# Performance work log

Hardware: AMD Instinct MI355X
Metric: run time of the kernel (lower is better)

## Reference

```python
import jax, jax.numpy as jnp
import numpy as np

B, N, PREV, PRED, H = 16, 64, 6, 30, 256
E = N * (N - 1)
BN_EPS = 1e-5


def _mlp(x, W1, b1, W2, b2, gamma, beta):
    # Two-layer ELU MLP with batch norm over flattened (batch*rows) dim.
    h = jax.nn.elu(x @ W1 + b1)
    h = jax.nn.elu(h @ W2 + b2)
    b, n, d = h.shape
    f = h.reshape(b * n, d)
    mu = f.mean(axis=0)
    var = f.var(axis=0)
    f = (f - mu) * jax.lax.rsqrt(var + BN_EPS) * gamma + beta
    return f.reshape(b, n, d)


def setup_inputs() -> dict:
    key = jax.random.key(0)
    ks = jax.random.split(key, 8)
    # fully-connected directed graph without self loops
    recv, send = np.where(~np.eye(N, dtype=bool))  # each [E]
    rel_rec = jnp.broadcast_to(jax.nn.one_hot(jnp.asarray(recv), N)[None], (B, E, N)).astype(jnp.float32)
    rel_send = jnp.broadcast_to(jax.nn.one_hot(jnp.asarray(send), N)[None], (B, E, N)).astype(jnp.float32)

    def xavier(k, shape):
        fan_in, fan_out = shape
        std = np.sqrt(2.0 / (fan_in + fan_out))
        return jax.random.normal(k, shape, jnp.float32) * std

    return {
        "prev_actor_centers": jax.random.normal(ks[0], (B, N, PREV, 2), jnp.float32) * 10.0,
        "rel_rec": rel_rec,
        "rel_send": rel_send,
        "W_traj": xavier(ks[1], (PREV * 2, H)),
        "b_traj": jnp.full((H,), 0.1, jnp.float32),
        "n2e_W1": xavier(ks[2], (2 * H, H)),
        "n2e_b1": jnp.full((H,), 0.1, jnp.float32),
        "n2e_W2": xavier(ks[3], (H, H)),
        "n2e_b2": jnp.full((H,), 0.1, jnp.float32),
        "n2e_gamma": jnp.ones((H,), jnp.float32),
        "n2e_beta": jnp.zeros((H,), jnp.float32),
        "e2n_W1": xavier(ks[4], (2 * H, H)),
        "e2n_b1": jnp.full((H,), 0.1, jnp.float32),
        "e2n_W2": xavier(ks[5], (H, H)),
        "e2n_b2": jnp.full((H,), 0.1, jnp.float32),
        "e2n_gamma": jnp.ones((H,), jnp.float32),
        "e2n_beta": jnp.zeros((H,), jnp.float32),
        "W_fuse": xavier(ks[6], (2 * H, H)),
        "b_fuse": jnp.full((H,), 0.1, jnp.float32),
        "W_pred": xavier(ks[7], (H, PRED * 2)),
        "b_pred": jnp.full((PRED * 2,), 0.1, jnp.float32),
    }


def reference(prev_actor_centers, rel_rec, rel_send,
              W_traj, b_traj,
              n2e_W1, n2e_b1, n2e_W2, n2e_b2, n2e_gamma, n2e_beta,
              e2n_W1, e2n_b1, e2n_W2, e2n_b2, e2n_gamma, e2n_beta,
              W_fuse, b_fuse, W_pred, b_pred):
    b, n, prev, _ = prev_actor_centers.shape
    # relative displacements, first step zero
    diffs = prev_actor_centers[:, :, 1:, :] - prev_actor_centers[:, :, :-1, :]
    rel_pos = jnp.concatenate([jnp.zeros((b, n, 1, 2), prev_actor_centers.dtype), diffs], axis=2)
    rel_pos = rel_pos.reshape(b, n, prev * 2)
    x = rel_pos @ W_traj + b_traj  # [b, n, H] node features

    # node2edge: gather via one-hot relation matmuls
    receivers = jnp.einsum('ben,bnh->beh', rel_rec, x)
    senders = jnp.einsum('ben,bnh->beh', rel_send, x)
    edges = jnp.concatenate([receivers, senders], axis=-1)  # [b, E, 2H]
    e = _mlp(edges, n2e_W1, n2e_b1, n2e_W2, n2e_b2, n2e_gamma, n2e_beta)

    # edge2node: degree-normalized scatter via transposed relation matmuls
    deg_rec = rel_rec.sum(axis=1)  # [b, n]
    deg_rec = deg_rec + (deg_rec == 0).astype(deg_rec.dtype)
    incoming = jnp.einsum('ben,beh->bnh', rel_rec, e) / deg_rec[..., None]
    deg_send = rel_send.sum(axis=1)
    deg_send = deg_send + (deg_send == 0).astype(deg_send.dtype)
    outgoing = jnp.einsum('ben,beh->bnh', rel_send, e) / deg_send[..., None]
    nodes = jnp.concatenate([incoming, outgoing], axis=-1)  # [b, n, 2H]
    m = _mlp(nodes, e2n_W1, e2n_b1, e2n_W2, e2n_b2, e2n_gamma, e2n_beta)

    fused = jnp.concatenate([x, m], axis=-1) @ W_fuse + b_fuse  # [b, n, H]
    rel = fused @ W_pred + b_pred  # [b, n, PRED*2]

    current_loc = prev_actor_centers[:, :, -1, :]  # [b, n, 2]
    current_loc = jnp.broadcast_to(current_loc[:, :, None, :], (b, n, PRED, 2)).reshape(b, n, PRED * 2)
    pos = jnp.cumsum(rel.reshape(b, n, PRED, 2), axis=2).reshape(b, n, PRED * 2) + current_loc
    return (rel, pos)
```

## Files before the change

### kernel.cpp

```cpp
#include <hip/hip_runtime.h>
#include <hip/hip_bf16.h>

#define BB 16
#define NN 64
#define PREVN 6
#define PREDN 30
#define HH 256
#define EE 4032
#define EROWS (BB*EE)
#define NROWS (BB*NN)

typedef short short8 __attribute__((ext_vector_type(8)));
typedef float f32x4 __attribute__((ext_vector_type(4)));

enum : int {
  OFF_STATS_E = 0,
  OFF_STATS_M = 1024,
  OFF_XRS     = 2048,
  F32_END     = 264192
};
enum : size_t {
  BO_W1TE  = 0,
  BO_W2TE  = 131072,
  BO_W1TN  = 196608,
  BO_W2TN  = 327680,
  BO_WFT   = 393216,
  BO_WPT   = 524288,
  BO_XG    = 540672,
  BO_NODES = 802816,
  BO_H1G   = 1327104,
  BO_M2    = 1589248,
  BO_FG    = 1851392,
  BO_E2    = 2113536
};

__device__ __forceinline__ float eluf(float v) { return v > 0.f ? v : __expf(v) - 1.f; }

__device__ __forceinline__ float xembed(const float* __restrict__ centers,
                                        const float* __restrict__ Wt,
                                        const float* __restrict__ bt,
                                        int rr, int col) {
  const float* c = centers + rr * 12;
  float acc = bt[col];
  #pragma unroll
  for (int t = 0; t < 5; ++t) {
    float dx = c[(t+1)*2 + 0] - c[t*2 + 0];
    float dy = c[(t+1)*2 + 1] - c[t*2 + 1];
    acc += dx * Wt[(2 + 2*t)*HH + col] + dy * Wt[(3 + 2*t)*HH + col];
  }
  return acc;
}

struct PrepArgs {
  const float *centers, *W_traj, *b_traj;
  const float *n2e_W1, *n2e_W2, *e2n_W1, *e2n_W2, *W_fuse, *W_pred;
  float* ws;
  float* inc;
  __hip_bfloat16 *p1e, *p2e, *p1n, *p2n, *pf, *pp, *xg;
};

__global__ __launch_bounds__(256) void k_prep(PrepArgs a) {
  const int bid = blockIdx.x, tid = threadIdx.x;
  if (bid < 264) {
    const float* W; __hip_bfloat16* P; int ksh, t0, pad = 0;
    if (bid < 64)       { W = a.n2e_W1; P = a.p1e; ksh = 4; t0 = bid*4; }
    else if (bid < 96)  { W = a.n2e_W2; P = a.p2e; ksh = 3; t0 = (bid-64)*4; }
    else if (bid < 160) { W = a.e2n_W1; P = a.p1n; ksh = 4; t0 = (bid-96)*4; }
    else if (bid < 192) { W = a.e2n_W2; P = a.p2n; ksh = 3; t0 = (bid-160)*4; }
    else if (bid < 256) { W = a.W_fuse; P = a.pf;  ksh = 4; t0 = (bid-192)*4; }
    else                { W = a.W_pred; P = a.pp;  ksh = 3; t0 = (bid-256)*4; pad = 1; }
    const int l = tid & 63, sub = tid >> 6;
    const int t = t0 + sub;
    const int j = t >> ksh, ks = t & ((1 << ksh) - 1);
    const int m16 = l & 15, q = l >> 4;
    __hip_bfloat16* dst = P + ((size_t)t*64 + l)*8;
    if (!pad) {
      const float* src = W + (size_t)(ks*32 + q*8)*256 + j*16 + m16;
      #pragma unroll
      for (int e = 0; e < 8; ++e)
        dst[e] = __float2bfloat16(src[(size_t)e*256]);
    } else {
      const int col = j*16 + m16;
      #pragma unroll
      for (int e = 0; e < 8; ++e)
        dst[e] = __float2bfloat16(col < 60 ?
                     W[(size_t)(ks*32 + q*8 + e)*60 + col] : 0.f);
    }
  } else if (bid < 272) {
    a.ws[(bid - 264) * 256 + tid] = 0.f;
  } else if (bid < 336) {
    int row0 = (bid - 272) * 16;
    #pragma unroll
    for (int r = 0; r < 16; ++r)
      a.xg[(size_t)(row0 + r)*256 + tid] =
          __float2bfloat16(xembed(a.centers, a.W_traj, a.b_traj, row0 + r, tid));
  } else {
    float* p = a.inc + (size_t)(bid - 336) * 4096;
    #pragma unroll
    for (int i = 0; i < 4; ++i)
      *reinterpret_cast<float4*>(p + (i*256 + tid)*4) = (float4){0.f,0.f,0.f,0.f};
  }
}

__global__ __launch_bounds__(64) void k_xrs2(
    const __hip_bfloat16* __restrict__ xg,
    const __hip_bfloat16* __restrict__ W1P,
    const float* __restrict__ b1,
    __hip_bfloat16* __restrict__ xrs) {
  const int lane = threadIdx.x;
  const int m16 = lane & 15, quad = lane >> 4;
  const int ko = quad * 8;
  const int rt = blockIdx.x >> 3, s = blockIdx.x & 7;
  const int half = s >> 2, j0 = (s & 3) * 64;
  const int jg0 = (s & 3) * 4;
  const int row0 = rt * 16;
  __hip_bfloat16* dst = xrs + (size_t)half * 262144;

  f32x4 acc[4];
  #pragma unroll
  for (int jt = 0; jt < 4; ++jt) {
    float bv = half ? 0.f : b1[j0 + jt*16 + m16];
    acc[jt] = (f32x4){bv, bv, bv, bv};
  }
  #pragma unroll
  for (int ks = 0; ks < 8; ++ks) {
    short8 af = *reinterpret_cast<const short8*>(
        xg + (size_t)(row0 + m16)*256 + ks*32 + ko);
    short8 bf[4];
    #pragma unroll
    for (int jt = 0; jt < 4; ++jt)
      bf[jt] = *reinterpret_cast<const short8*>(
          W1P + (((size_t)(jg0 + jt)*16 + half*8 + ks)*64 + lane)*8);
    #pragma unroll
    for (int jt = 0; jt < 4; ++jt)
      acc[jt] = __builtin_amdgcn_mfma_f32_16x16x32_bf16(af, bf[jt], acc[jt], 0, 0, 0);
  }
  #pragma unroll
  for (int jt = 0; jt < 4; ++jt)
    #pragma unroll
    for (int r = 0; r < 4; ++r)
      dst[(size_t)(row0 + quad*4 + r)*256 + j0 + jt*16 + m16] =
          __float2bfloat16(acc[jt][r]);
}

__global__ __launch_bounds__(256, 4) void k_mlp8(
    const __hip_bfloat16* __restrict__ xrs,
    const __hip_bfloat16* __restrict__ W2P,
    const float* __restrict__ b2,
    __hip_bfloat16* __restrict__ outp,
    float* __restrict__ stats,
    float* __restrict__ incraw) {
  __shared__ alignas(16) __hip_bfloat16 h1s[64][264];
  __shared__ float sst[3][256];
  const int tid = threadIdx.x;
  const int w = tid >> 6, lane = tid & 63;
  const int m16 = lane & 15, quad = lane >> 4;
  const int ko = quad * 8;
  const int blk = blockIdx.x;
  const int bb = blk / 63, lb = blk - bb*63;
  const int n0 = (lb * 64) / 63;
  const int thr = (n0 + 1) * 63 - lb * 64;
  const int colw = w * 64;

  #pragma unroll
  for (int i = 0; i < 3; ++i) sst[i][tid] = 0.f;

  {
    const int rg = tid >> 5;
    const int c8 = (tid & 31) * 8;
    const __hip_bfloat16* xrb = xrs + (size_t)(bb*64 + n0)*256 + c8;
    const __hip_bfloat16* xsb = xrs + 262144 + (size_t)bb*64*256 + c8;
    union { uint4 u; __hip_bfloat16 h[8]; } vr0, vr1;
    vr0.u = *reinterpret_cast<const uint4*>(xrb);
    vr1.u = *reinterpret_cast<const uint4*>(xrb + 256);
    #pragma unroll
    for (int i = 0; i < 8; ++i) {
      int r = rg + i*8;
      int isn1 = (r >= thr) ? 1 : 0;
      int rc = n0 + isn1;
      int jj = lb*64 + r - rc*63;
      int sd = jj + (jj >= rc ? 1 : 0);
      union { uint4 u; __hip_bfloat16 h[8]; } vs, va, o;
      vs.u = *reinterpret_cast<const uint4*>(xsb + (size_t)sd*256);
      va.u = isn1 ? vr1.u : vr0.u;
      #pragma unroll
      for (int j = 0; j < 8; ++j)
        o.h[j] = __float2bfloat16(eluf(__bfloat162float(va.h[j]) +
                                       __bfloat162float(vs.h[j])));
      *reinterpret_cast<uint4*>(&h1s[r][c8]) = o.u;
    }
  }
  __syncthreads();

  f32x4 acc2[4][4];
  #pragma unroll
  for (int jt = 0; jt < 4; ++jt) {
    float bv = b2[colw + jt*16 + m16];
    #pragma unroll
    for (int mt = 0; mt < 4; ++mt) acc2[mt][jt] = (f32x4){bv, bv, bv, bv};
  }
  #pragma unroll
  for (int kt = 0; kt < 4; ++kt) {
    #pragma unroll
    for (int ks = 0; ks < 2; ++ks) {
      const int k0 = kt*64 + ks*32 + ko;
      const int chunk = kt*2 + ks;
      short8 af[4], bf[4];
      #pragma unroll
      for (int jt = 0; jt < 4; ++jt)
        bf[jt] = *reinterpret_cast<const short8*>(
            W2P + (((size_t)(w*4 + jt)*8 + chunk)*64 + lane)*8);
      #pragma unroll
      for (int mt = 0; mt < 4; ++mt)
        af[mt] = *(const short8*)((const char*)h1s +
                     (size_t)(mt*16 + m16)*528 + k0*2);
      #pragma unroll
      for (int mt = 0; mt < 4; ++mt)
        #pragma unroll
        for (int jt = 0; jt < 4; ++jt)
          acc2[mt][jt] = __builtin_amdgcn_mfma_f32_16x16x32_bf16(af[mt], bf[jt],
                                                                 acc2[mt][jt], 0, 0, 0);
    }
  }
  __syncthreads();

  #pragma unroll
  for (int jt = 0; jt < 4; ++jt) {
    float s0 = 0.f, s1 = 0.f, sq = 0.f;
    #pragma unroll
    for (int mt = 0; mt < 4; ++mt)
      #pragma unroll
      for (int r = 0; r < 4; ++r) {
        int row = mt*16 + quad*4 + r;
        float hv = eluf(acc2[mt][jt][r]);
        h1s[row][colw + jt*16 + m16] = __float2bfloat16(hv);
        float t1 = (row >= thr) ? hv : 0.f;
        s1 += t1; s0 += hv - t1;
        sq += hv * hv;
      }
    atomicAdd(&sst[0][colw + jt*16 + m16], s0);
    atomicAdd(&sst[1][colw + jt*16 + m16], s1);
    atomicAdd(&sst[2][colw + jt*16 + m16], sq);
  }
  __syncthreads();

  {
    float s0 = sst[0][tid], s1 = sst[1][tid];
    atomicAdd(&stats[tid], s0 + s1);
    atomicAdd(&stats[256 + tid], sst[2][tid]);
    atomicAdd(&incraw[(size_t)(bb*64 + n0)*256 + tid], s0);
    atomicAdd(&incraw[(size_t)(bb*64 + n0 + 1)*256 + tid], s1);
  }
  #pragma unroll
  for (int i = 0; i < 8; ++i) {
    int u = i*256 + tid;
    int r = u >> 5, c = (u & 31) * 8;
    int isn1 = (r >= thr) ? 1 : 0;
    int rc = n0 + isn1;
    int jj = lb*64 + r - rc*63;
    int sd = jj + (jj >= rc ? 1 : 0);
    int jpos = rc - (jj < rc ? 1 : 0);
    *reinterpret_cast<uint4*>(outp + ((size_t)(bb*64 + sd)*63 + jpos)*HH + c) =
        *reinterpret_cast<const uint4*>(&h1s[r][c]);
  }
}

__global__ __launch_bounds__(256) void k_aggS(const __hip_bfloat16* __restrict__ e2,
                                              const float* __restrict__ incraw,
                                              const float* __restrict__ st,
                                              const float* __restrict__ gam,
                                              const float* __restrict__ bet,
                                              __hip_bfloat16* __restrict__ nodes) {
  __shared__ float red[8][256];
  const int bn = blockIdx.x;
  const int tid = threadIdx.x;
  const int c8 = (tid & 31) * 8;
  const int rg = tid >> 5;
  const __hip_bfloat16* base = e2 + (size_t)bn * 63 * HH;
  float s[8] = {0.f,0.f,0.f,0.f,0.f,0.f,0.f,0.f};
  for (int j = rg; j < 63; j += 8) {
    union { uint4 u; __hip_bfloat16 h[8]; } v;
    v.u = *reinterpret_cast<const uint4*>(base + (size_t)j*HH + c8);
    #pragma unroll
    for (int jj = 0; jj < 8; ++jj) s[jj] += __bfloat162float(v.h[jj]);
  }
  #pragma unroll
  for (int jj = 0; jj < 8; jj += 4)
    *reinterpret_cast<float4*>(&red[rg][c8 + jj]) =
        (float4){s[jj], s[jj+1], s[jj+2], s[jj+3]};
  __syncthreads();
  float S = 0.f;
  #pragma unroll
  for (int r = 0; r < 8; ++r) S += red[r][tid];
  const float inv = 1.f / (float)EROWS;
  float mean = st[tid] * inv;
  float var  = fmaxf(st[256 + tid] * inv - mean*mean, 0.f);
  float a = gam[tid] * rsqrtf(var + 1e-5f);
  float c0 = bet[tid] - mean * a;
  float in_v  = a * (incraw[(size_t)bn*256 + tid] * (1.f/63.f)) + c0;
  float out_v = a * (S * (1.f/63.f)) + c0;
  nodes[(size_t)bn*512 + tid]       = __float2bfloat16(in_v);
  nodes[(size_t)bn*512 + 256 + tid] = __float2bfloat16(out_v);
}

__global__ __launch_bounds__(64) void k_n1(
    const __hip_bfloat16* __restrict__ nodes,
    const __hip_bfloat16* __restrict__ W1P,
    const float* __restrict__ b1,
    __hip_bfloat16* __restrict__ h1g) {
  __shared__ alignas(16) __hip_bfloat16 hls[16][40];
  const int lane = threadIdx.x;
  const int m16 = lane & 15, quad = lane >> 4;
  const int ko = quad * 8;
  const int row0 = (blockIdx.x >> 3) * 16;
  const int jb = blockIdx.x & 7;
  const int j0 = jb * 32;

  f32x4 acc[2];
  #pragma unroll
  for (int jt = 0; jt < 2; ++jt) {
    float bv = b1[j0 + jt*16 + m16];
    acc[jt] = (f32x4){bv, bv, bv, bv};
  }
  #pragma unroll
  for (int ks = 0; ks < 16; ++ks) {
    short8 af = *reinterpret_cast<const short8*>(
        nodes + (size_t)(row0 + m16)*512 + ks*32 + ko);
    short8 bf[2];
    #pragma unroll
    for (int jt = 0; jt < 2; ++jt)
      bf[jt] = *reinterpret_cast<const short8*>(
          W1P + (((size_t)(jb*2 + jt)*16 + ks)*64 + lane)*8);
    #pragma unroll
    for (int jt = 0; jt < 2; ++jt)
      acc[jt] = __builtin_amdgcn_mfma_f32_16x16x32_bf16(af, bf[jt], acc[jt], 0, 0, 0);
  }
  #pragma unroll
  for (int jt = 0; jt < 2; ++jt)
    #pragma unroll
    for (int r = 0; r < 4; ++r)
      hls[quad*4 + r][jt*16 + m16] = __float2bfloat16(eluf(acc[jt][r]));
  {
    int r = lane >> 2, c = (lane & 3) * 8;
    *reinterpret_cast<uint4*>(h1g + (size_t)(row0 + r)*256 + j0 + c) =
        *reinterpret_cast<const uint4*>(&hls[r][c]);
  }
}

__global__ __launch_bounds__(64) void k_n2(
    const __hip_bfloat16* __restrict__ h1g,
    const __hip_bfloat16* __restrict__ W2P,
    const float* __restrict__ b2,
    __hip_bfloat16* __restrict__ m2,
    float* __restrict__ stats) {
  __shared__ alignas(16) __hip_bfloat16 hls[16][40];
  __shared__ float sst[2][32];
  const int lane = threadIdx.x;
  const int m16 = lane & 15, quad = lane >> 4;
  const int ko = quad * 8;
  const int row0 = (blockIdx.x >> 3) * 16;
  const int jb = blockIdx.x & 7;
  const int j0 = jb * 32;

  if (lane < 32) { sst[0][lane] = 0.f; sst[1][lane] = 0.f; }

  f32x4 acc[2];
  #pragma unroll
  for (int jt = 0; jt < 2; ++jt) {
    float bv = b2[j0 + jt*16 + m16];
    acc[jt] = (f32x4){bv, bv, bv, bv};
  }
  #pragma unroll
  for (int ks = 0; ks < 8; ++ks) {
    short8 af = *reinterpret_cast<const short8*>(
        h1g + (size_t)(row0 + m16)*256 + ks*32 + ko);
    short8 bf[2];
    #pragma unroll
    for (int jt = 0; jt < 2; ++jt)
      bf[jt] = *reinterpret_cast<const short8*>(
          W2P + (((size_t)(jb*2 + jt)*8 + ks)*64 + lane)*8);
    #pragma unroll
    for (int jt = 0; jt < 2; ++jt)
      acc[jt] = __builtin_amdgcn_mfma_f32_16x16x32_bf16(af, bf[jt], acc[jt], 0, 0, 0);
  }
  #pragma unroll
  for (int jt = 0; jt < 2; ++jt) {
    float ps = 0.f, pq = 0.f;
    #pragma unroll
    for (int r = 0; r < 4; ++r) {
      float hv = eluf(acc[jt][r]);
      hls[quad*4 + r][jt*16 + m16] = __float2bfloat16(hv);
      ps += hv; pq += hv * hv;
    }
    atomicAdd(&sst[0][jt*16 + m16], ps);
    atomicAdd(&sst[1][jt*16 + m16], pq);
  }
  if (lane < 32) {
    atomicAdd(&stats[j0 + lane], sst[0][lane]);
    atomicAdd(&stats[256 + j0 + lane], sst[1][lane]);
  }
  {
    int r = lane >> 2, c = (lane & 3) * 8;
    *reinterpret_cast<uint4*>(m2 + (size_t)(row0 + r)*256 + j0 + c) =
        *reinterpret_cast<const uint4*>(&hls[r][c]);
  }
}

__global__ __launch_bounds__(64) void k_hf(
    const __hip_bfloat16* __restrict__ xg,
    const __hip_bfloat16* __restrict__ m2,
    const float* __restrict__ stM,
    const float* __restrict__ gam,
    const float* __restrict__ bet,
    const __hip_bfloat16* __restrict__ WfP,
    const float* __restrict__ bfv,
    __hip_bfloat16* __restrict__ fg) {
  __shared__ alignas(16) __hip_bfloat16 hls[16][40];
  __shared__ float bnA[256], bnC[256];
  const int lane = threadIdx.x;
  const int m16 = lane & 15, quad = lane >> 4;
  const int ko = quad * 8;
  const int row0 = (blockIdx.x >> 3) * 16;
  const int jb = blockIdx.x & 7;
  const int j0 = jb * 32;

  {
    const float inv = 1.f / (float)NROWS;
    #pragma unroll
    for (int j = 0; j < 4; ++j) {
      int k = lane*4 + j;
      float mean = stM[k] * inv;
      float var  = fmaxf(stM[256 + k] * inv - mean*mean, 0.f);
      float am = gam[k] * rsqrtf(var + 1e-5f);
      bnA[k] = am;
      bnC[k] = bet[k] - mean * am;
    }
  }

  f32x4 acc[2];
  #pragma unroll
  for (int jt = 0; jt < 2; ++jt) {
    float bv = bfv[j0 + jt*16 + m16];
    acc[jt] = (f32x4){bv, bv, bv, bv};
  }
  #pragma unroll
  for (int ks = 0; ks < 16; ++ks) {
    short8 af;
    if (ks < 8) {
      af = *reinterpret_cast<const short8*>(
          xg + (size_t)(row0 + m16)*256 + ks*32 + ko);
    } else {
      int k0 = (ks - 8)*32 + ko;
      union { uint4 u; __hip_bfloat16 h[8]; } v;
      v.u = *reinterpret_cast<const uint4*>(m2 + (size_t)(row0 + m16)*256 + k0);
      union { short8 s8; __hip_bfloat16 h[8]; } o;
      #pragma unroll
      for (int j = 0; j < 8; ++j)
        o.h[j] = __float2bfloat16(bnA[k0+j] * __bfloat162float(v.h[j]) + bnC[k0+j]);
      af = o.s8;
    }
    short8 bf[2];
    #pragma unroll
    for (int jt = 0; jt < 2; ++jt)
      bf[jt] = *reinterpret_cast<const short8*>(
          WfP + (((size_t)(jb*2 + jt)*16 + ks)*64 + lane)*8);
    #pragma unroll
    for (int jt = 0; jt < 2; ++jt)
      acc[jt] = __builtin_amdgcn_mfma_f32_16x16x32_bf16(af, bf[jt], acc[jt], 0, 0, 0);
  }
  #pragma unroll
  for (int jt = 0; jt < 2; ++jt)
    #pragma unroll
    for (int r = 0; r < 4; ++r)
      hls[quad*4 + r][jt*16 + m16] = __float2bfloat16(acc[jt][r]);
  {
    int r = lane >> 2, c = (lane & 3) * 8;
    *reinterpret_cast<uint4*>(fg + (size_t)(row0 + r)*256 + j0 + c) =
        *reinterpret_cast<const uint4*>(&hls[r][c]);
  }
}

__global__ __launch_bounds__(64) void k_pred(
    const __hip_bfloat16* __restrict__ fg,
    const __hip_bfloat16* __restrict__ WpP,
    const float* __restrict__ bp,
    const float* __restrict__ centers,
    float* __restrict__ out) {
  __shared__ float rl[16][68];
  const int lane = threadIdx.x;
  const int m16 = lane & 15, quad = lane >> 4;
  const int ko = quad * 8;
  const int row0 = blockIdx.x * 16;

  f32x4 acc[4];
  #pragma unroll
  for (int jt = 0; jt < 4; ++jt) {
    int c = jt*16 + m16;
    float bv = (c < 60) ? bp[c] : 0.f;
    acc[jt] = (f32x4){bv, bv, bv, bv};
  }
  #pragma unroll
  for (int ks = 0; ks < 8; ++ks) {
    short8 af = *reinterpret_cast<const short8*>(
        fg + (size_t)(row0 + m16)*256 + ks*32 + ko);
    short8 bf[4];
    #pragma unroll
    for (int jt = 0; jt < 4; ++jt)
      bf[jt] = *reinterpret_cast<const short8*>(
          WpP + (((size_t)jt*8 + ks)*64 + lane)*8);
    #pragma unroll
    for (int jt = 0; jt < 4; ++jt)
      acc[jt] = __builtin_amdgcn_mfma_f32_16x16x32_bf16(af, bf[jt], acc[jt], 0, 0, 0);
  }
  #pragma unroll
  for (int jt = 0; jt < 4; ++jt) {
    int c = jt*16 + m16;
    #pragma unroll
    for (int r = 0; r < 4; ++r) {
      int lr = quad*4 + r;
      rl[lr][c] = acc[jt][r];
      if (c < 60) out[(size_t)(row0 + lr)*60 + c] = acc[jt][r];
    }
  }
  if (lane < 32) {
    int lr = lane >> 1, xy = lane & 1;
    int grow = row0 + lr;
    float run = centers[(size_t)(grow*PREVN + 5)*2 + xy];
    #pragma unroll
    for (int p = 0; p < PREDN; ++p) {
      run += rl[lr][2*p + xy];
      out[61440 + (size_t)grow*60 + 2*p + xy] = run;
    }
  }
}

extern "C" void kernel_launch(void* const* d_in, const int* in_sizes, int n_in,
                              void* d_out, int out_size, void* d_ws, size_t ws_size,
                              hipStream_t stream) {
  const float* centers = (const float*)d_in[0];
  float* ws = (float*)d_ws;
  __hip_bfloat16* wb = (__hip_bfloat16*)(ws + F32_END);
  __hip_bfloat16* xrs = (__hip_bfloat16*)(ws + OFF_XRS);
  float* incraw = (float*)(wb + BO_H1G);

  const float* W_traj = (const float*)d_in[3];
  const float* b_traj = (const float*)d_in[4];
  const float* n2e_b1 = (const float*)d_in[6];
  const float* n2e_b2 = (const float*)d_in[8];
  const float* n2e_g  = (const float*)d_in[9];
  const float* n2e_be = (const float*)d_in[10];
  const float* e2n_b1 = (const float*)d_in[12];
  const float* e2n_b2 = (const float*)d_in[14];
  const float* e2n_g  = (const float*)d_in[15];
  const float* e2n_be = (const float*)d_in[16];
  const float* b_fuse = (const float*)d_in[18];
  const float* b_pred = (const float*)d_in[20];

  PrepArgs pa;
  pa.centers = centers; pa.W_traj = W_traj; pa.b_traj = b_traj;
  pa.n2e_W1 = (const float*)d_in[5];  pa.n2e_W2 = (const float*)d_in[7];
  pa.e2n_W1 = (const float*)d_in[11]; pa.e2n_W2 = (const float*)d_in[13];
  pa.W_fuse = (const float*)d_in[17]; pa.W_pred = (const float*)d_in[19];
  pa.ws = ws; pa.inc = incraw;
  pa.p1e = wb + BO_W1TE; pa.p2e = wb + BO_W2TE;
  pa.p1n = wb + BO_W1TN; pa.p2n = wb + BO_W2TN;
  pa.pf = wb + BO_WFT;   pa.pp = wb + BO_WPT;
  pa.xg = wb + BO_XG;

  k_prep<<<400, 256, 0, stream>>>(pa);
  k_xrs2<<<512, 64, 0, stream>>>(wb + BO_XG, wb + BO_W1TE, n2e_b1, xrs);
  k_mlp8<<<EROWS/64, 256, 0, stream>>>(xrs, wb + BO_W2TE, n2e_b2, wb + BO_E2,
                                       ws + OFF_STATS_E, incraw);
  k_aggS<<<NROWS, 256, 0, stream>>>(wb + BO_E2, incraw, ws + OFF_STATS_E,
                                    n2e_g, n2e_be, wb + BO_NODES);
  k_n1<<<512, 64, 0, stream>>>(wb + BO_NODES, wb + BO_W1TN, e2n_b1, wb + BO_H1G);
  k_n2<<<512, 64, 0, stream>>>(wb + BO_H1G, wb + BO_W2TN, e2n_b2, wb + BO_M2,
                               ws + OFF_STATS_M);
  k_hf<<<512, 64, 0, stream>>>(wb + BO_XG, wb + BO_M2, ws + OFF_STATS_M,
                               e2n_g, e2n_be, wb + BO_WFT, b_fuse, wb + BO_FG);
  k_pred<<<64, 64, 0, stream>>>(wb + BO_FG, wb + BO_WPT, b_pred, centers,
                                (float*)d_out);
}
```

Baseline: 195.2 us.

## Fuse node-stage kernels into one persistent kernel with grid-wide barrier

Replaces five node-side kernels (aggregation, two e2n MLP layers, fuse, pred) with a single 256-block kernel. Each block handles 4 nodes and keeps its intermediates in shared memory instead of global buffers. An atomic counter acts as a grid-wide barrier so the batch-norm statistics of the second MLP are complete before the fuse layer runs. This removes launch overhead and global round trips, but each MFMA tile is 16 rows wide while only 4 rows are valid, so most of that matrix work is wasted. It also relies on all blocks being resident at once, and on the counter being reset between calls, which is not visible here.

```diff
diff --git a/kernel.cpp b/kernel.cpp
--- a/kernel.cpp
+++ b/kernel.cpp
@@ -16,6 +16,7 @@
 enum : int {
   OFF_STATS_E = 0,
   OFF_STATS_M = 1024,
+  OFF_CNT     = 1536,
   OFF_XRS     = 2048,
   F32_END     = 264192
 };
@@ -27,10 +28,7 @@
   BO_WFT   = 393216,
   BO_WPT   = 524288,
   BO_XG    = 540672,
-  BO_NODES = 802816,
-  BO_H1G   = 1327104,
-  BO_M2    = 1589248,
-  BO_FG    = 1851392,
+  BO_INC   = 802816,
   BO_E2    = 2113536
 };
 
@@ -265,271 +263,228 @@
   }
 }
 
-__global__ __launch_bounds__(256) void k_aggS(const __hip_bfloat16* __restrict__ e2,
-                                              const float* __restrict__ incraw,
-                                              const float* __restrict__ st,
-                                              const float* __restrict__ gam,
-                                              const float* __restrict__ bet,
-                                              __hip_bfloat16* __restrict__ nodes) {
-  __shared__ float red[8][256];
-  const int bn = blockIdx.x;
+struct NodeArgs {
+  const __hip_bfloat16 *e2;
+  const float *incraw;
+  const float *stE, *gamE, *betE;
+  const __hip_bfloat16 *W1P; const float *b1;
+  const __hip_bfloat16 *W2P; const float *b2;
+  float *stM; const float *gamM, *betM;
+  const __hip_bfloat16 *WfP; const float *bfv;
+  const __hip_bfloat16 *WpP; const float *bp;
+  const __hip_bfloat16 *xg;
+  const float *centers;
+  unsigned int *cnt;
+  float *out;
+};
+
+__global__ __launch_bounds__(256) void k_node(NodeArgs a) {
+  __shared__ alignas(16) __hip_bfloat16 nds[16][520];
+  __shared__ alignas(16) __hip_bfloat16 h1[16][264];
+  __shared__ alignas(16) __hip_bfloat16 m2[16][264];
+  __shared__ alignas(16) __hip_bfloat16 fgs[16][264];
+  __shared__ float bnv[2][256];
+  __shared__ float rl[4][68];
   const int tid = threadIdx.x;
-  const int c8 = (tid & 31) * 8;
-  const int rg = tid >> 5;
-  const __hip_bfloat16* base = e2 + (size_t)bn * 63 * HH;
-  float s[8] = {0.f,0.f,0.f,0.f,0.f,0.f,0.f,0.f};
-  for (int j = rg; j < 63; j += 8) {
-    union { uint4 u; __hip_bfloat16 h[8]; } v;
-    v.u = *reinterpret_cast<const uint4*>(base + (size_t)j*HH + c8);
-    #pragma unroll
-    for (int jj = 0; jj < 8; ++jj) s[jj] += __bfloat162float(v.h[jj]);
-  }
-  #pragma unroll
-  for (int jj = 0; jj < 8; jj += 4)
-    *reinterpret_cast<float4*>(&red[rg][c8 + jj]) =
-        (float4){s[jj], s[jj+1], s[jj+2], s[jj+3]};
-  __syncthreads();
-  float S = 0.f;
-  #pragma unroll
-  for (int r = 0; r < 8; ++r) S += red[r][tid];
-  const float inv = 1.f / (float)EROWS;
-  float mean = st[tid] * inv;
-  float var  = fmaxf(st[256 + tid] * inv - mean*mean, 0.f);
-  float a = gam[tid] * rsqrtf(var + 1e-5f);
-  float c0 = bet[tid] - mean * a;
-  float in_v  = a * (incraw[(size_t)bn*256 + tid] * (1.f/63.f)) + c0;
-  float out_v = a * (S * (1.f/63.f)) + c0;
-  nodes[(size_t)bn*512 + tid]       = __float2bfloat16(in_v);
-  nodes[(size_t)bn*512 + 256 + tid] = __float2bfloat16(out_v);
-}
-
-__global__ __launch_bounds__(64) void k_n1(
-    const __hip_bfloat16* __restrict__ nodes,
-    const __hip_bfloat16* __restrict__ W1P,
-    const float* __restrict__ b1,
-    __hip_bfloat16* __restrict__ h1g) {
-  __shared__ alignas(16) __hip_bfloat16 hls[16][40];
-  const int lane = threadIdx.x;
+  const int w = tid >> 6, lane = tid & 63;
   const int m16 = lane & 15, quad = lane >> 4;
   const int ko = quad * 8;
-  const int row0 = (blockIdx.x >> 3) * 16;
-  const int jb = blockIdx.x & 7;
-  const int j0 = jb * 32;
-
-  f32x4 acc[2];
-  #pragma unroll
-  for (int jt = 0; jt < 2; ++jt) {
-    float bv = b1[j0 + jt*16 + m16];
-    acc[jt] = (f32x4){bv, bv, bv, bv};
-  }
-  #pragma unroll
-  for (int ks = 0; ks < 16; ++ks) {
-    short8 af = *reinterpret_cast<const short8*>(
-        nodes + (size_t)(row0 + m16)*512 + ks*32 + ko);
-    short8 bf[2];
-    #pragma unroll
-    for (int jt = 0; jt < 2; ++jt)
-      bf[jt] = *reinterpret_cast<const short8*>(
-          W1P + (((size_t)(jb*2 + jt)*16 + ks)*64 + lane)*8);
-    #pragma unroll
-    for (int jt = 0; jt < 2; ++jt)
-      acc[jt] = __builtin_amdgcn_mfma_f32_16x16x32_bf16(af, bf[jt], acc[jt], 0, 0, 0);
-  }
-  #pragma unroll
-  for (int jt = 0; jt < 2; ++jt)
-    #pragma unroll
-    for (int r = 0; r < 4; ++r)
-      hls[quad*4 + r][jt*16 + m16] = __float2bfloat16(eluf(acc[jt][r]));
-  {
-    int r = lane >> 2, c = (lane & 3) * 8;
-    *reinterpret_cast<uint4*>(h1g + (size_t)(row0 + r)*256 + j0 + c) =
-        *reinterpret_cast<const uint4*>(&hls[r][c]);
-  }
-}
-
-__global__ __launch_bounds__(64) void k_n2(
-    const __hip_bfloat16* __restrict__ h1g,
-    const __hip_bfloat16* __restrict__ W2P,
-    const float* __restrict__ b2,
-    __hip_bfloat16* __restrict__ m2,
-    float* __restrict__ stats) {
-  __shared__ alignas(16) __hip_bfloat16 hls[16][40];
-  __shared__ float sst[2][32];
-  const int lane = threadIdx.x;
-  const int m16 = lane & 15, quad = lane >> 4;
-  const int ko = quad * 8;
-  const int row0 = (blockIdx.x >> 3) * 16;
-  const int jb = blockIdx.x & 7;
-  const int j0 = jb * 32;
-
-  if (lane < 32) { sst[0][lane] = 0.f; sst[1][lane] = 0.f; }
-
-  f32x4 acc[2];
-  #pragma unroll
-  for (int jt = 0; jt < 2; ++jt) {
-    float bv = b2[j0 + jt*16 + m16];
-    acc[jt] = (f32x4){bv, bv, bv, bv};
-  }
-  #pragma unroll
-  for (int ks = 0; ks < 8; ++ks) {
-    short8 af = *reinterpret_cast<const short8*>(
-        h1g + (size_t)(row0 + m16)*256 + ks*32 + ko);
-    short8 bf[2];
-    #pragma unroll
-    for (int jt = 0; jt < 2; ++jt)
-      bf[jt] = *reinterpret_cast<const short8*>(
-          W2P + (((size_t)(jb*2 + jt)*8 + ks)*64 + lane)*8);
-    #pragma unroll
-    for (int jt = 0; jt < 2; ++jt)
-      acc[jt] = __builtin_amdgcn_mfma_f32_16x16x32_bf16(af, bf[jt], acc[jt], 0, 0, 0);
-  }
-  #pragma unroll
-  for (int jt = 0; jt < 2; ++jt) {
-    float ps = 0.f, pq = 0.f;
-    #pragma unroll
-    for (int r = 0; r < 4; ++r) {
-      float hv = eluf(acc[jt][r]);
-      hls[quad*4 + r][jt*16 + m16] = __float2bfloat16(hv);
-      ps += hv; pq += hv * hv;
-    }
-    atomicAdd(&sst[0][jt*16 + m16], ps);
-    atomicAdd(&sst[1][jt*16 + m16], pq);
-  }
+  const int bn0 = blockIdx.x * 4;
+
+  {
+    const float inv = 1.f / (float)EROWS;
+    float mean = a.stE[tid] * inv;
+    float var  = fmaxf(a.stE[256 + tid] * inv - mean*mean, 0.f);
+    float am = a.gamE[tid] * rsqrtf(var + 1e-5f);
+    bnv[0][tid] = am;
+    bnv[1][tid] = a.betE[tid] - mean * am;
+  }
+  {
+    unsigned int* z = reinterpret_cast<unsigned int*>(&nds[4][0]);
+    for (int i = tid; i < 12*260; i += 256) z[i] = 0u;
+  }
+
+  const int rw = lane >> 5, c8 = (lane & 31) * 8;
+  float s[8] = {0.f,0.f,0.f,0.f,0.f,0.f,0.f,0.f};
+  {
+    const __hip_bfloat16* ebase = a.e2 + ((size_t)(bn0 + w) * 63) * HH + c8;
+    #pragma unroll 4
+    for (int k = 0; k < 32; ++k) {
+      int row = rw + 2*k;
+      if (row < 63) {
+        union { uint4 u; __hip_bfloat16 h[8]; } v;
+        v.u = *reinterpret_cast<const uint4*>(ebase + (size_t)row * HH);
+        #pragma unroll
+        for (int j = 0; j < 8; ++j) s[j] += __bfloat162float(v.h[j]);
+      }
+    }
+    #pragma unroll
+    for (int j = 0; j < 8; ++j) s[j] += __shfl_xor(s[j], 32);
+  }
+  __syncthreads();
   if (lane < 32) {
-    atomicAdd(&stats[j0 + lane], sst[0][lane]);
-    atomicAdd(&stats[256 + j0 + lane], sst[1][lane]);
-  }
-  {
-    int r = lane >> 2, c = (lane & 3) * 8;
-    *reinterpret_cast<uint4*>(m2 + (size_t)(row0 + r)*256 + j0 + c) =
-        *reinterpret_cast<const uint4*>(&hls[r][c]);
-  }
-}
-
-__global__ __launch_bounds__(64) void k_hf(
-    const __hip_bfloat16* __restrict__ xg,
-    const __hip_bfloat16* __restrict__ m2,
-    const float* __restrict__ stM,
-    const float* __restrict__ gam,
-    const float* __restrict__ bet,
-    const __hip_bfloat16* __restrict__ WfP,
-    const float* __restrict__ bfv,
-    __hip_bfloat16* __restrict__ fg) {
-  __shared__ alignas(16) __hip_bfloat16 hls[16][40];
-  __shared__ float bnA[256], bnC[256];
-  const int lane = threadIdx.x;
-  const int m16 = lane & 15, quad = lane >> 4;
-  const int ko = quad * 8;
-  const int row0 = (blockIdx.x >> 3) * 16;
-  const int jb = blockIdx.x & 7;
-  const int j0 = jb * 32;
+    const float* ip = a.incraw + (size_t)(bn0 + w)*256 + c8;
+    #pragma unroll
+    for (int j = 0; j < 8; ++j) {
+      int col = c8 + j;
+      float am = bnv[0][col], c0 = bnv[1][col];
+      nds[w][col]       = __float2bfloat16(am * (ip[j] * (1.f/63.f)) + c0);
+      nds[w][256 + col] = __float2bfloat16(am * (s[j]  * (1.f/63.f)) + c0);
+    }
+  }
+  __syncthreads();
+
+  {
+    f32x4 acc[4];
+    #pragma unroll
+    for (int jt = 0; jt < 4; ++jt) {
+      float bv = a.b1[w*64 + jt*16 + m16];
+      acc[jt] = (f32x4){bv, bv, bv, bv};
+    }
+    #pragma unroll
+    for (int ks = 0; ks < 16; ++ks) {
+      short8 af = *reinterpret_cast<const short8*>(&nds[m16][ks*32 + ko]);
+      short8 bf[4];
+      #pragma unroll
+      for (int jt = 0; jt < 4; ++jt)
+        bf[jt] = *reinterpret_cast<const short8*>(
+            a.W1P + (((size_t)(w*4 + jt)*16 + ks)*64 + lane)*8);
+      #pragma unroll
+      for (int jt = 0; jt < 4; ++jt)
+        acc[jt] = __builtin_amdgcn_mfma_f32_16x16x32_bf16(af, bf[jt], acc[jt], 0, 0, 0);
+    }
+    #pragma unroll
+    for (int jt = 0; jt < 4; ++jt)
+      #pragma unroll
+      for (int r = 0; r < 4; ++r)
+        h1[quad*4 + r][w*64 + jt*16 + m16] = __float2bfloat16(eluf(acc[jt][r]));
+  }
+  __syncthreads();
+
+  {
+    f32x4 acc[4];
+    #pragma unroll
+    for (int jt = 0; jt < 4; ++jt) {
+      float bv = a.b2[w*64 + jt*16 + m16];
+      acc[jt] = (f32x4){bv, bv, bv, bv};
+    }
+    #pragma unroll
+    for (int ks = 0; ks < 8; ++ks) {
+      short8 af = *(const short8*)((const char*)h1 +
+                      (size_t)m16*528 + (ks*32 + ko)*2);
+      short8 bf[4];
+      #pragma unroll
+      for (int jt = 0; jt < 4; ++jt)
+        bf[jt] = *reinterpret_cast<const short8*>(
+            a.W2P + (((size_t)(w*4 + jt)*8 + ks)*64 + lane)*8);
+      #pragma unroll
+      for (int jt = 0; jt < 4; ++jt)
+        acc[jt] = __builtin_amdgcn_mfma_f32_16x16x32_bf16(af, bf[jt], acc[jt], 0, 0, 0);
+    }
+    #pragma unroll
+    for (int jt = 0; jt < 4; ++jt) {
+      float ps = 0.f, pq = 0.f;
+      #pragma unroll
+      for (int r = 0; r < 4; ++r) {
+        float hv = eluf(acc[jt][r]);
+        m2[quad*4 + r][w*64 + jt*16 + m16] = __float2bfloat16(hv);
+        ps += hv; pq += hv * hv;
+      }
+      if (quad == 0) {
+        int col = w*64 + jt*16 + m16;
+        atomicAdd(&a.stM[col], ps);
+        atomicAdd(&a.stM[256 + col], pq);
+      }
+    }
+  }
+  __syncthreads();
+  __threadfence();
+  if (tid == 0) {
+    __hip_atomic_fetch_add(a.cnt, 1u, __ATOMIC_ACQ_REL, __HIP_MEMORY_SCOPE_AGENT);
+    while (__hip_atomic_load(a.cnt, __ATOMIC_ACQUIRE, __HIP_MEMORY_SCOPE_AGENT) < 256u)
+      __builtin_amdgcn_s_sleep(2);
+  }
+  __syncthreads();
 
   {
     const float inv = 1.f / (float)NROWS;
-    #pragma unroll
-    for (int j = 0; j < 4; ++j) {
-      int k = lane*4 + j;
-      float mean = stM[k] * inv;
-      float var  = fmaxf(stM[256 + k] * inv - mean*mean, 0.f);
-      float am = gam[k] * rsqrtf(var + 1e-5f);
-      bnA[k] = am;
-      bnC[k] = bet[k] - mean * am;
-    }
-  }
-
-  f32x4 acc[2];
-  #pragma unroll
-  for (int jt = 0; jt < 2; ++jt) {
-    float bv = bfv[j0 + jt*16 + m16];
-    acc[jt] = (f32x4){bv, bv, bv, bv};
-  }
-  #pragma unroll
-  for (int ks = 0; ks < 16; ++ks) {
-    short8 af;
-    if (ks < 8) {
-      af = *reinterpret_cast<const short8*>(
-          xg + (size_t)(row0 + m16)*256 + ks*32 + ko);
-    } else {
-      int k0 = (ks - 8)*32 + ko;
-      union { uint4 u; __hip_bfloat16 h[8]; } v;
-      v.u = *reinterpret_cast<const uint4*>(m2 + (size_t)(row0 + m16)*256 + k0);
-      union { short8 s8; __hip_bfloat16 h[8]; } o;
-      #pragma unroll
-      for (int j = 0; j < 8; ++j)
-        o.h[j] = __float2bfloat16(bnA[k0+j] * __bfloat162float(v.h[j]) + bnC[k0+j]);
-      af = o.s8;
-    }
-    short8 bf[2];
-    #pragma unroll
-    for (int jt = 0; jt < 2; ++jt)
-      bf[jt] = *reinterpret_cast<const short8*>(
-          WfP + (((size_t)(jb*2 + jt)*16 + ks)*64 + lane)*8);
-    #pragma unroll
-    for (int jt = 0; jt < 2; ++jt)
-      acc[jt] = __builtin_amdgcn_mfma_f32_16x16x32_bf16(af, bf[jt], acc[jt], 0, 0, 0);
-  }
-  #pragma unroll
-  for (int jt = 0; jt < 2; ++jt)
-    #pragma unroll
-    for (int r = 0; r < 4; ++r)
-      hls[quad*4 + r][jt*16 + m16] = __float2bfloat16(acc[jt][r]);
-  {
-    int r = lane >> 2, c = (lane & 3) * 8;
-    *reinterpret_cast<uint4*>(fg + (size_t)(row0 + r)*256 + j0 + c) =
-        *reinterpret_cast<const uint4*>(&hls[r][c]);
-  }
-}
-
-__global__ __launch_bounds__(64) void k_pred(
-    const __hip_bfloat16* __restrict__ fg,
-    const __hip_bfloat16* __restrict__ WpP,
-    const float* __restrict__ bp,
-    const float* __restrict__ centers,
-    float* __restrict__ out) {
-  __shared__ float rl[16][68];
-  const int lane = threadIdx.x;
-  const int m16 = lane & 15, quad = lane >> 4;
-  const int ko = quad * 8;
-  const int row0 = blockIdx.x * 16;
-
-  f32x4 acc[4];
-  #pragma unroll
-  for (int jt = 0; jt < 4; ++jt) {
-    int c = jt*16 + m16;
-    float bv = (c < 60) ? bp[c] : 0.f;
-    acc[jt] = (f32x4){bv, bv, bv, bv};
-  }
-  #pragma unroll
-  for (int ks = 0; ks < 8; ++ks) {
-    short8 af = *reinterpret_cast<const short8*>(
-        fg + (size_t)(row0 + m16)*256 + ks*32 + ko);
-    short8 bf[4];
+    float mean = a.stM[tid] * inv;
+    float var  = fmaxf(a.stM[256 + tid] * inv - mean*mean, 0.f);
+    float am = a.gamM[tid] * rsqrtf(var + 1e-5f);
+    bnv[0][tid] = am;
+    bnv[1][tid] = a.betM[tid] - mean * am;
+  }
+  __syncthreads();
+
+  {
+    f32x4 acc[4];
+    #pragma unroll
+    for (int jt = 0; jt < 4; ++jt) {
+      float bv = a.bfv[w*64 + jt*16 + m16];
+      acc[jt] = (f32x4){bv, bv, bv, bv};
+    }
+    #pragma unroll
+    for (int ks = 0; ks < 16; ++ks) {
+      short8 af;
+      if (ks < 8) {
+        af = *reinterpret_cast<const short8*>(
+            a.xg + (size_t)(bn0 + m16)*256 + ks*32 + ko);
+      } else {
+        int k0 = (ks - 8)*32 + ko;
+        union { short8 s8; __hip_bfloat16 h[8]; } o;
+        #pragma unroll
+        for (int j = 0; j < 8; ++j) {
+          float mv = __bfloat162float(m2[m16][k0 + j]);
+          o.h[j] = __float2bfloat16(bnv[0][k0+j] * mv + bnv[1][k0+j]);
+        }
+        af = o.s8;
+      }
+      short8 bf[4];
+      #pragma unroll
+      for (int jt = 0; jt < 4; ++jt)
+        bf[jt] = *reinterpret_cast<const short8*>(
+            a.WfP + (((size_t)(w*4 + jt)*16 + ks)*64 + lane)*8);
+      #pragma unroll
+      for (int jt = 0; jt < 4; ++jt)
+        acc[jt] = __builtin_amdgcn_mfma_f32_16x16x32_bf16(af, bf[jt], acc[jt], 0, 0, 0);
+    }
     #pragma unroll
     for (int jt = 0; jt < 4; ++jt)
-      bf[jt] = *reinterpret_cast<const short8*>(
-          WpP + (((size_t)jt*8 + ks)*64 + lane)*8);
-    #pragma unroll
-    for (int jt = 0; jt < 4; ++jt)
-      acc[jt] = __builtin_amdgcn_mfma_f32_16x16x32_bf16(af, bf[jt], acc[jt], 0, 0, 0);
-  }
-  #pragma unroll
-  for (int jt = 0; jt < 4; ++jt) {
-    int c = jt*16 + m16;
-    #pragma unroll
-    for (int r = 0; r < 4; ++r) {
-      int lr = quad*4 + r;
-      rl[lr][c] = acc[jt][r];
-      if (c < 60) out[(size_t)(row0 + lr)*60 + c] = acc[jt][r];
-    }
-  }
-  if (lane < 32) {
-    int lr = lane >> 1, xy = lane & 1;
-    int grow = row0 + lr;
-    float run = centers[(size_t)(grow*PREVN + 5)*2 + xy];
+      #pragma unroll
+      for (int r = 0; r < 4; ++r)
+        fgs[quad*4 + r][w*64 + jt*16 + m16] = __float2bfloat16(acc[jt][r]);
+  }
+  __syncthreads();
+
+  {
+    int c = w*16 + m16;
+    float bv = (c < 60) ? a.bp[c] : 0.f;
+    f32x4 acc = (f32x4){bv, bv, bv, bv};
+    #pragma unroll
+    for (int ks = 0; ks < 8; ++ks) {
+      short8 af = *(const short8*)((const char*)fgs +
+                      (size_t)m16*528 + (ks*32 + ko)*2);
+      short8 bf = *reinterpret_cast<const short8*>(
+          a.WpP + (((size_t)w*8 + ks)*64 + lane)*8);
+      acc = __builtin_amdgcn_mfma_f32_16x16x32_bf16(af, bf, acc, 0, 0, 0);
+    }
+    if (quad == 0) {
+      #pragma unroll
+      for (int r = 0; r < 4; ++r) {
+        rl[r][c] = acc[r];
+        if (c < 60) a.out[(size_t)(bn0 + r)*60 + c] = acc[r];
+      }
+    }
+  }
+  __syncthreads();
+  if (tid < 8) {
+    int lr = tid >> 1, xy = tid & 1;
+    int grow = bn0 + lr;
+    float run = a.centers[(size_t)(grow*PREVN + 5)*2 + xy];
     #pragma unroll
     for (int p = 0; p < PREDN; ++p) {
       run += rl[lr][2*p + xy];
-      out[61440 + (size_t)grow*60 + 2*p + xy] = run;
+      a.out[61440 + (size_t)grow*60 + 2*p + xy] = run;
     }
   }
 }
@@ -541,7 +496,7 @@
   float* ws = (float*)d_ws;
   __hip_bfloat16* wb = (__hip_bfloat16*)(ws + F32_END);
   __hip_bfloat16* xrs = (__hip_bfloat16*)(ws + OFF_XRS);
-  float* incraw = (float*)(wb + BO_H1G);
+  float* incraw = (float*)(wb + BO_INC);
 
   const float* W_traj = (const float*)d_in[3];
   const float* b_traj = (const float*)d_in[4];
@@ -571,13 +526,16 @@
   k_xrs2<<<512, 64, 0, stream>>>(wb + BO_XG, wb + BO_W1TE, n2e_b1, xrs);
   k_mlp8<<<EROWS/64, 256, 0, stream>>>(xrs, wb + BO_W2TE, n2e_b2, wb + BO_E2,
                                        ws + OFF_STATS_E, incraw);
-  k_aggS<<<NROWS, 256, 0, stream>>>(wb + BO_E2, incraw, ws + OFF_STATS_E,
-                                    n2e_g, n2e_be, wb + BO_NODES);
-  k_n1<<<512, 64, 0, stream>>>(wb + BO_NODES, wb + BO_W1TN, e2n_b1, wb + BO_H1G);
-  k_n2<<<512, 64, 0, stream>>>(wb + BO_H1G, wb + BO_W2TN, e2n_b2, wb + BO_M2,
-                               ws + OFF_STATS_M);
-  k_hf<<<512, 64, 0, stream>>>(wb + BO_XG, wb + BO_M2, ws + OFF_STATS_M,
-                               e2n_g, e2n_be, wb + BO_WFT, b_fuse, wb + BO_FG);
-  k_pred<<<64, 64, 0, stream>>>(wb + BO_FG, wb + BO_WPT, b_pred, centers,
-                                (float*)d_out);
+  NodeArgs na;
+  na.e2 = wb + BO_E2; na.incraw = incraw;
+  na.stE = ws + OFF_STATS_E; na.gamE = n2e_g; na.betE = n2e_be;
+  na.W1P = wb + BO_W1TN; na.b1 = e2n_b1;
+  na.W2P = wb + BO_W2TN; na.b2 = e2n_b2;
+  na.stM = ws + OFF_STATS_M; na.gamM = e2n_g; na.betM = e2n_be;
+  na.WfP = wb + BO_WFT; na.bfv = b_fuse;
+  na.WpP = wb + BO_WPT; na.bp = b_pred;
+  na.xg = wb + BO_XG; na.centers = centers;
+  na.cnt = (unsigned int*)(ws + OFF_CNT);
+  na.out = (float*)d_out;
+  k_node<<<256, 256, 0, stream>>>(na);
 }
```

Result: slower. 220.0 us (+12.7%).
